# Performance work log

Measured on AMD Instinct MI355X. Metric: run time of the kernel, lower is better.

## Reference

```python
import jax, jax.numpy as jnp
import numpy as np

B, N, E, H, L, T, IN = 32, 512, 32768, 64, 2, 2, 8
TAU = 0.5


def setup_inputs() -> dict:
    key = jax.random.key(0)
    ks = jax.random.split(key, 32)
    f = lambda i, shape, s=0.05: jax.random.normal(ks[i], shape, jnp.float32) * s
    u = jax.random.uniform(ks[3], (B, E, T), jnp.float32, 1e-6, 1.0 - 1e-6)
    return {
        "inputs": f(0, (B, N, IN), 1.0),
        "hidden": f(1, (B, N, H), 1.0),
        "edge_logits": f(2, (B, E, T), 1.0),
        "gumbel": -jnp.log(-jnp.log(u)),  # standard Gumbel noise (deterministic here)
        "send_edges": jax.random.randint(ks[4], (E,), 0, N),
        "recv_edges": jax.random.randint(ks[5], (E,), 0, N),
        "W1": f(6, (L, T, H, 2 * H)), "b1": f(7, (L, T, H)),
        "W2": f(8, (L, T, H, H)), "b2": f(9, (L, T, H)),
        "Whr": f(10, (H, L * H)), "Whi": f(11, (H, L * H)), "Whh": f(12, (H, L * H)),
        "Wir": f(13, (H, IN)), "bir": f(14, (H,)),
        "Wii": f(15, (H, IN)), "bii": f(16, (H,)),
        "Win": f(17, (H, IN)), "bin_w": f(18, (H,)),
        "Wm1": f(19, (H, H)), "bm1": f(20, (H,)),
        "Wm2": f(21, (H, H)), "bm2": f(22, (H,)),
        "Wdf": f(23, (N, N * H), 0.005), "bdf": f(24, (N,)),
        "Wloc": f(25, (N, N * H), 0.005), "bloc": f(26, (N,)),
        "Wscale": f(27, (N, N * H), 0.005), "bscale": f(28, (N,)),
    }


def _lin(x, W, b):
    return jnp.einsum('...i,oi->...o', x, W) + b


def reference(inputs, hidden, edge_logits, gumbel, send_edges, recv_edges,
              W1, b1, W2, b2, Whr, Whi, Whh,
              Wir, bir, Wii, bii, Win, bin_w,
              Wm1, bm1, Wm2, bm2,
              Wdf, bdf, Wloc, bloc, Wscale, bscale):
    # hard gumbel-softmax (straight-through)
    y_soft = jax.nn.softmax((edge_logits + gumbel) / TAU, axis=-1)
    y_hard = jax.nn.one_hot(jnp.argmax(y_soft, axis=-1), T, dtype=y_soft.dtype)
    edges = jax.lax.stop_gradient(y_hard - y_soft) + y_soft  # [B,E,T]

    # normalized receiver degree (zeros -> 1), as in edge2node_mat / degree
    deg = jnp.zeros((N,), jnp.float32).at[recv_edges].add(1.0)
    deg = jnp.where(deg == 0, 1.0, deg)

    hidden_ = hidden
    aggs = []
    norm = float(T)  # skip_first_edge_type=False
    for k in range(L):
        pre = jnp.concatenate([hidden_[:, recv_edges], hidden_[:, send_edges]], axis=-1)  # [B,E,2H]
        all_msgs = jnp.zeros((B, E, H), pre.dtype)
        for t in range(T):  # per-edge-type tanh MLP (eval mode: dropout off)
            m = jnp.tanh(jnp.einsum('bef,hf->beh', pre, W1[k, t]) + b1[k, t])
            m = jnp.tanh(jnp.einsum('beh,gh->beg', m, W2[k, t]) + b2[k, t])
            all_msgs = all_msgs + m * edges[:, :, t:t + 1] / norm
        # scatter-mean onto receiver nodes (= normalized edge2node matmul)
        agg = jnp.zeros((B, N, H), all_msgs.dtype).at[:, recv_edges].add(all_msgs) / deg[None, :, None]
        hidden_ = agg
        aggs.append(agg)
    agg = jnp.concatenate(aggs, axis=-1)  # [B,N,L*H]

    r = jax.nn.sigmoid(_lin(inputs, Wir, bir) + jnp.einsum('bnf,of->bno', agg, Whr))
    i = jax.nn.sigmoid(_lin(inputs, Wii, bii) + jnp.einsum('bnf,of->bno', agg, Whi))
    n = jnp.tanh(_lin(inputs, Win, bin_w) + r * jnp.einsum('bnf,of->bno', agg, Whh))
    hidden_new = (1.0 - i) * n + i * hidden  # [B,N,H]

    pred = _lin(jax.nn.relu(_lin(hidden_new, Wm1, bm1)), Wm2, bm2)
    flat = pred.reshape(B, -1)  # [B, N*H]
    df = 2.0 + jax.nn.softplus(flat @ Wdf.T + bdf)      # StudentT domain maps
    loc = flat @ Wloc.T + bloc
    scale = jax.nn.softplus(flat @ Wscale.T + bscale)
    return df, loc, scale, hidden_new, edges
```

## Files before the change

### kernel.cpp

```cpp
#include <hip/hip_runtime.h>

#define B_  32
#define N_  512
#define E_  32768
#define H_  64
#define L_  2
#define T_  2
#define IN_ 8

typedef __attribute__((ext_vector_type(4))) float f32x4;
typedef __attribute__((ext_vector_type(8))) short bf16x8;
typedef __attribute__((ext_vector_type(4))) short s16x4;
typedef __attribute__((ext_vector_type(4))) unsigned u32x4;

__device__ __forceinline__ short f2bf(float f){
  unsigned u = __float_as_uint(f);
  u += 0x7FFFu + ((u >> 16) & 1u);
  return (short)(u >> 16);
}
__device__ __forceinline__ float bf2f(short s){
  return __uint_as_float(((unsigned)(unsigned short)s) << 16);
}
__device__ __forceinline__ bf16x8 pack8(f32x4 a, f32x4 b){
  bf16x8 r;
  r[0]=f2bf(a[0]); r[1]=f2bf(a[1]); r[2]=f2bf(a[2]); r[3]=f2bf(a[3]);
  r[4]=f2bf(b[0]); r[5]=f2bf(b[1]); r[6]=f2bf(b[2]); r[7]=f2bf(b[3]);
  return r;
}
__device__ __forceinline__ float lo16f(unsigned u){ return __uint_as_float(u << 16); }
__device__ __forceinline__ float hi16f(unsigned u){ return __uint_as_float(u & 0xffff0000u); }

__device__ __forceinline__ float fast_tanh(float x){
  float e = __builtin_amdgcn_exp2f(x * 2.8853900817779268f);
  float r = __builtin_amdgcn_rcpf(e + 1.0f);
  return __builtin_fmaf(-2.0f, r, 1.0f);
}
__device__ __forceinline__ float fast_sigm(float x){
  return __builtin_amdgcn_rcpf(1.0f + __builtin_amdgcn_exp2f(x * -1.4426950408889634f));
}
__device__ __forceinline__ float softplus_f(float x){
  return fmaxf(x, 0.0f) + log1pf(__expf(-fabsf(x)));
}

__global__ void k_edges(const float* __restrict__ logits, const float* __restrict__ gum,
                        float* __restrict__ edges_out, unsigned char* __restrict__ type_out){
  int i = blockIdx.x * 256 + threadIdx.x;
  if(i >= B_ * E_) return;
  float l0 = logits[2*i]   + gum[2*i];
  float l1 = logits[2*i+1] + gum[2*i+1];
  int t = (l1 > l0) ? 1 : 0;
  edges_out[2*i]   = t ? 0.f : 1.f;
  edges_out[2*i+1] = t ? 1.f : 0.f;
  type_out[i] = (unsigned char)t;
}

__global__ void k_hist(const int* __restrict__ recvE, int* __restrict__ hist){
  int e = blockIdx.x * 256 + threadIdx.x;
  if(e < E_) atomicAdd(&hist[recvE[e]], 1);
}
__global__ void k_scan(const int* __restrict__ hist, int* __restrict__ row_start,
                       float* __restrict__ deg){
  __shared__ int a[512], bbuf[512];
  int t = threadIdx.x;
  int h = hist[t];
  a[t] = h;
  __syncthreads();
  int* cur = a; int* nxt = bbuf;
  for(int off = 1; off < 512; off <<= 1){
    int v = cur[t] + (t >= off ? cur[t - off] : 0);
    nxt[t] = v;
    __syncthreads();
    int* tmp = cur; cur = nxt; nxt = tmp;
  }
  row_start[t] = cur[t] - h;
  if(t == 0) row_start[512] = E_;
  deg[t] = (h == 0) ? 1.0f : (float)h;
}

__global__ void k_hist2(const int* __restrict__ recvE, const unsigned char* __restrict__ typ,
                        int* __restrict__ n0){
  __shared__ int lh[512];
  int b = blockIdx.y, tid = threadIdx.x;
  lh[tid] = 0; lh[tid + 256] = 0;
  __syncthreads();
  int e0 = blockIdx.x * 2048;
  for(int k = 0; k < 8; ++k){
    int e = e0 + k*256 + tid;
    if(typ[(size_t)b*E_ + e] == 0) atomicAdd(&lh[recvE[e]], 1);
  }
  __syncthreads();
  if(lh[tid])       atomicAdd(&n0[b*512 + tid],       lh[tid]);
  if(lh[tid + 256]) atomicAdd(&n0[b*512 + tid + 256], lh[tid + 256]);
}
__global__ void k_scan2(const int* __restrict__ n0, const int* __restrict__ row_start,
                        int* __restrict__ stt){
  __shared__ int a[512], bbuf[512];
  __shared__ int tot;
  int b = blockIdx.x, t = threadIdx.x;
  int h = n0[b*512 + t];
  a[t] = h;
  __syncthreads();
  int* cur = a; int* nxt = bbuf;
  for(int off = 1; off < 512; off <<= 1){
    int v = cur[t] + (t >= off ? cur[t - off] : 0);
    nxt[t] = v;
    __syncthreads();
    int* tmp = cur; cur = nxt; nxt = tmp;
  }
  if(t == 511) tot = cur[511];
  __syncthreads();
  int excl = cur[t] - h;
  stt[(b*2    )*513 + t] = excl;
  stt[(b*2 + 1)*513 + t] = tot + row_start[t] - excl;
  if(t == 0){ stt[(b*2)*513 + 512] = tot; stt[(b*2+1)*513 + 512] = E_; }
}
__global__ void k_perm2(const int* __restrict__ recvE, const unsigned char* __restrict__ typ,
                        const int* __restrict__ stt, int* __restrict__ cur0,
                        int* __restrict__ cur1, unsigned short* __restrict__ perm2){
  int i = blockIdx.x * 256 + threadIdx.x;
  int b = i >> 15, e = i & (E_ - 1);
  int r = recvE[e];
  int pos;
  if(typ[i] == 0) pos = stt[(b*2  )*513 + r] + atomicAdd(&cur0[b*512 + r], 1);
  else            pos = stt[(b*2+1)*513 + r] + atomicAdd(&cur1[b*512 + r], 1);
  perm2[(size_t)b*E_ + pos] = (unsigned short)e;
}

__launch_bounds__(256, 2)
__global__ void k_prep(const float* __restrict__ hid,
                       const float* __restrict__ W1, const float* __restrict__ b1,
                       unsigned short* __restrict__ P, int layer){
  __shared__ __align__(16) short WT[256 * 64];
  __shared__ float bias[256];
  __shared__ float hidl[32 * 64];

  const int tid = threadIdx.x;
  const int b   = blockIdx.y;
  const int nbase = blockIdx.x * 32;
  const float* W1k = W1 + layer * (T_ * H_ * 2 * H_);

  {
    int col = tid, slot = col >> 6, h = col & 63;
    int t = slot & 1, prt = slot >> 1;
    const float* src = W1k + t*8192 + h*128 + prt*64;
#pragma unroll
    for(int u = 0; u < 8; ++u){
      bf16x8 v = pack8(*(const f32x4*)(src + u*8), *(const f32x4*)(src + u*8 + 4));
      int bo = col*128 + ((u*16) ^ ((col & 7) << 4));
      *(bf16x8*)((char*)WT + bo) = v;
    }
    bias[col] = (slot < 2) ? b1[layer*128 + t*64 + h] : 0.0f;
  }
  {
    const float* src = hid + ((size_t)b*N_ + nbase)*H_;
    ((f32x4*)hidl)[tid]       = ((const f32x4*)src)[tid];
    ((f32x4*)hidl)[tid + 256] = ((const f32x4*)src)[tid + 256];
  }
  __syncthreads();

  const int col = tid;
  for(int n = 0; n < 32; ++n){
    const float* hrow = hidl + n*64;
    float acc = bias[col];
#pragma unroll
    for(int u = 0; u < 8; ++u){
      int bo = col*128 + ((u*16) ^ ((col & 7) << 4));
      bf16x8 wv = *(const bf16x8*)((const char*)WT + bo);
#pragma unroll
      for(int i = 0; i < 8; ++i) acc += hrow[u*8 + i] * bf2f(wv[i]);
    }
    P[(((size_t)b*N_ + nbase + n) << 8) + col] = (unsigned short)f2bf(acc);
  }
}

__launch_bounds__(256, 5)
__global__ void k_msg(const unsigned short* __restrict__ P,
                      const float* __restrict__ W2, const float* __restrict__ b2,
                      const int* __restrict__ recvE, const int* __restrict__ sendE,
                      const unsigned short* __restrict__ perm2,
                      const int* __restrict__ stt, const float* __restrict__ deg,
                      float* __restrict__ agg, int layer){
  __shared__ __align__(16) short m1_lds[2][64 * 64];
  __shared__ float acc[8][64];
  __shared__ float b2_lds[128];
  __shared__ short rl_lds[2][64];

  const int tid  = threadIdx.x;
  const int w    = tid >> 6, lane = tid & 63;
  const int l15  = lane & 15, l4 = lane >> 4;
  const int b    = blockIdx.y;
  const int nodeBase = blockIdx.x * 8;

  const float* W2k = W2 + layer * (T_ * H_ * H_);

  if(tid < 128) b2_lds[tid] = b2[layer*128 + tid];
  acc[tid >> 6][tid & 63] = 0.0f;
  { int t2 = tid + 256; acc[t2 >> 6][t2 & 63] = 0.0f; }

  bf16x8 B2f[2][2];
#pragma unroll
  for(int t = 0; t < 2; ++t)
#pragma unroll
    for(int ks = 0; ks < 2; ++ks){
      const float* p = W2k + (t*64 + w*16 + l15)*64 + ks*32 + l4*8;
      B2f[t][ks] = pack8(*(const f32x4*)p, *(const f32x4*)(p+4));
    }

  const int gcol = w*16 + l15;
  const unsigned short* permB = perm2 + (size_t)b * E_;
  const int* sttB = stt + b*2*513;
  const int s0a = sttB[nodeBase],       s1a = sttB[nodeBase + 8];
  const int s0b = sttB[513 + nodeBase], s1b = sttB[513 + nodeBase + 8];
  const int nt0 = (s1a - s0a + 63) >> 6;
  const int nt  = nt0 + ((s1b - s0b + 63) >> 6);

  const int el = tid >> 2, part = tid & 3;
  const int h0 = part * 16;
  const int bo0 = el*128 + ((h0*2)      ^ ((el & 7) << 4));
  const int bo1 = el*128 + ((h0*2 + 16) ^ ((el & 7) << 4));

#define TILE_SL(t, sv, lv) { if((t) < nt0){ sv = s0a + (t)*64 + el; lv = s1a; } \
                             else { sv = s0b + ((t) - nt0)*64 + el; lv = s1b; } }

  u32x4 G0 = {}, G1 = {}, G2 = {}, G3 = {};
  int rl_cur = 255, eidA = 0;
  bool v_cur = false;

  if(nt > 0){
    int s, lim;
    TILE_SL(0, s, lim);
    bool v0 = s < lim;
    int e0 = v0 ? (int)permB[s] : 0;
    int rv0 = v0 ? recvE[e0] : 0;
    int sd0 = v0 ? sendE[e0] : 0;
    if(v0){
      int sg0 = (nt0 == 0) ? 1 : 0;
      const unsigned short* pr = P + (((size_t)b*N_ + rv0) << 8) + sg0*64 + h0;
      const unsigned short* ps = P + (((size_t)b*N_ + sd0) << 8) + (2 + sg0)*64 + h0;
      G0 = *(const u32x4*)pr; G1 = *(const u32x4*)(pr + 8);
      G2 = *(const u32x4*)ps; G3 = *(const u32x4*)(ps + 8);
    }
    rl_cur = v0 ? (rv0 - nodeBase) : 255;
    v_cur = v0;
    TILE_SL(1, s, lim);
    eidA = (s < lim) ? (int)permB[s] : 0;
  }

  for(int ti = 0; ti < nt; ++ti){
    const int c = ti & 1;
    if(v_cur){
      unsigned q0[4], q1[4];
#pragma unroll
      for(int j = 0; j < 4; ++j){
        unsigned t0 = (unsigned)(unsigned short)f2bf(fast_tanh(lo16f(G0[j]) + lo16f(G2[j])));
        unsigned t1 = (unsigned)(unsigned short)f2bf(fast_tanh(hi16f(G0[j]) + hi16f(G2[j])));
        q0[j] = t0 | (t1 << 16);
        unsigned t2 = (unsigned)(unsigned short)f2bf(fast_tanh(lo16f(G1[j]) + lo16f(G3[j])));
        unsigned t3 = (unsigned)(unsigned short)f2bf(fast_tanh(hi16f(G1[j]) + hi16f(G3[j])));
        q1[j] = t2 | (t3 << 16);
      }
      *(u32x4*)((char*)m1_lds[c] + bo0) = (u32x4){q0[0], q0[1], q0[2], q0[3]};
      *(u32x4*)((char*)m1_lds[c] + bo1) = (u32x4){q1[0], q1[1], q1[2], q1[3]};
    }else{
      u32x4 z = {};
      *(u32x4*)((char*)m1_lds[c] + bo0) = z;
      *(u32x4*)((char*)m1_lds[c] + bo1) = z;
    }
    if(part == 0) rl_lds[c][el] = (short)rl_cur;
    __syncthreads();

    int rvN = 0, sdN = 0; bool vN;
    {
      int s, lim;
      TILE_SL(ti + 1, s, lim);
      vN = s < lim;
      if(vN){ rvN = recvE[eidA]; sdN = sendE[eidA]; }
      TILE_SL(ti + 2, s, lim);
      eidA = (s < lim) ? (int)permB[s] : 0;
    }

    const int sg = (ti >= nt0) ? 1 : 0;
    f32x4 C2[4];
    { float bv = b2_lds[sg*64 + gcol];
#pragma unroll
      for(int ef = 0; ef < 4; ++ef) C2[ef] = (f32x4){bv, bv, bv, bv}; }
#pragma unroll
    for(int ks = 0; ks < 2; ++ks){
#pragma unroll
      for(int ef = 0; ef < 4; ++ef){
        int e = ef*16 + l15;
        int byteoff = e*128 + (((ks*32 + l4*8)*2) ^ ((e & 7) << 4));
        bf16x8 A = *(const bf16x8*)((const char*)m1_lds[c] + byteoff);
        C2[ef] = __builtin_amdgcn_mfma_f32_16x16x32_bf16(A, B2f[sg][ks], C2[ef], 0, 0, 0);
      }
    }
    {
      int prl = -1; float pend = 0.f;
#pragma unroll
      for(int ef = 0; ef < 4; ++ef){
        s16x4 rl4 = *(const s16x4*)&rl_lds[c][ef*16 + l4*4];
#pragma unroll
        for(int r = 0; r < 4; ++r){
          int rl = rl4[r];
          if(rl != prl){
            if(prl >= 0) atomicAdd(&acc[prl][gcol], pend);
            pend = 0.f;
            prl = (rl == 255) ? -1 : rl;
          }
          if(rl != 255) pend += fast_tanh(C2[ef][r]);
        }
      }
      if(prl >= 0) atomicAdd(&acc[prl][gcol], pend);
    }

    if(vN){
      const int sgN = (ti + 1 >= nt0) ? 1 : 0;
      const unsigned short* pr = P + (((size_t)b*N_ + rvN) << 8) + sgN*64 + h0;
      const unsigned short* ps = P + (((size_t)b*N_ + sdN) << 8) + (2 + sgN)*64 + h0;
      G0 = *(const u32x4*)pr; G1 = *(const u32x4*)(pr + 8);
      G2 = *(const u32x4*)ps; G3 = *(const u32x4*)(ps + 8);
    }else{
      G0 = (u32x4){}; G1 = (u32x4){}; G2 = (u32x4){}; G3 = (u32x4){};
    }
    rl_cur = vN ? (rvN - nodeBase) : 255;
    v_cur = vN;
  }
#undef TILE_SL
  __syncthreads();

#pragma unroll
  for(int q = 0; q < 2; ++q){
    int idx = tid + q*256;
    int rl = idx >> 6, g = idx & 63;
    int node = nodeBase + rl;
    agg[(((size_t)b*N_ + node) << 6) + g] = acc[rl][g] * 0.5f / deg[node];
  }
}

__launch_bounds__(256, 2)
__global__ void k_gru(const float* __restrict__ x, const float* __restrict__ hid,
                      const float* __restrict__ agg0, const float* __restrict__ agg1,
                      const float* __restrict__ Whr, const float* __restrict__ Whi,
                      const float* __restrict__ Whh,
                      const float* __restrict__ Wir, const float* __restrict__ bir,
                      const float* __restrict__ Wii, const float* __restrict__ bii,
                      const float* __restrict__ Win, const float* __restrict__ binw,
                      float* __restrict__ hnew){
  __shared__ short WhrT[128*64], WhiT[128*64], WhhT[128*64];
  __shared__ float WxT[3][8*64];
  __shared__ float bias[3][64];
  __shared__ float agg_lds[4][128];

  int tid = threadIdx.x;
  for(int s = tid; s < 8192; s += 256){
    int g = s >> 7, f = s & 127;
    WhrT[f*64+g] = f2bf(Whr[s]);
    WhiT[f*64+g] = f2bf(Whi[s]);
    WhhT[f*64+g] = f2bf(Whh[s]);
  }
  for(int s = tid; s < 512; s += 256){
    int g = s >> 3, j = s & 7;
    WxT[0][j*64+g] = Wir[s]; WxT[1][j*64+g] = Wii[s]; WxT[2][j*64+g] = Win[s];
  }
  if(tid < 64){ bias[0][tid] = bir[tid]; bias[1][tid] = bii[tid]; bias[2][tid] = binw[tid]; }
  __syncthreads();

  int w = tid >> 6, lane = tid & 63;
  for(int j = 0; j < 8; ++j){
    int id = blockIdx.x*32 + j*4 + w;
    size_t base = (size_t)id * 64;
    agg_lds[w][lane]      = agg0[base + lane];
    agg_lds[w][64 + lane] = agg1[base + lane];

    float ar = bias[0][lane], ai = bias[1][lane], an = bias[2][lane], ah = 0.f;
    const float* xp = x + (size_t)id * 8;
#pragma unroll
    for(int jj = 0; jj < 8; ++jj){
      float xv = xp[jj];
      ar += xv * WxT[0][jj*64+lane];
      ai += xv * WxT[1][jj*64+lane];
      an += xv * WxT[2][jj*64+lane];
    }
#pragma unroll 4
    for(int f = 0; f < 128; ++f){
      float av = agg_lds[w][f];
      ar += av * bf2f(WhrT[f*64+lane]);
      ai += av * bf2f(WhiT[f*64+lane]);
      ah += av * bf2f(WhhT[f*64+lane]);
    }
    float r  = fast_sigm(ar);
    float ii = fast_sigm(ai);
    float ng = fast_tanh(an + r * ah);
    float ho = hid[base + lane];
    hnew[base + lane] = (1.0f - ii) * ng + ii * ho;
  }
}

__launch_bounds__(256, 2)
__global__ void k_pred(const float* __restrict__ hnew,
                       const float* __restrict__ Wm1, const float* __restrict__ bm1,
                       const float* __restrict__ Wm2, const float* __restrict__ bm2,
                       unsigned short* __restrict__ flatbf){
  __shared__ float W1T[64*64], W2T[64*64];
  __shared__ float bias1[64], bias2[64];
  __shared__ float h_lds[4][64], t_lds[4][64];
  int tid = threadIdx.x;
  for(int s = tid; s < 4096; s += 256){
    int g = s >> 6, h = s & 63;
    W1T[h*64+g] = Wm1[s];
    W2T[h*64+g] = Wm2[s];
  }
  if(tid < 64){ bias1[tid] = bm1[tid]; bias2[tid] = bm2[tid]; }
  __syncthreads();

  int w = tid >> 6, lane = tid & 63;
  for(int j = 0; j < 8; ++j){
    int id = blockIdx.x*32 + j*4 + w;
    size_t base = (size_t)id * 64;
    h_lds[w][lane] = hnew[base + lane];
    float a = bias1[lane];
#pragma unroll 4
    for(int h = 0; h < 64; ++h) a += h_lds[w][h] * W1T[h*64+lane];
    a = fmaxf(a, 0.0f);
    t_lds[w][lane] = a;
    float p = bias2[lane];
#pragma unroll 4
    for(int h = 0; h < 64; ++h) p += t_lds[w][h] * W2T[h*64+lane];
    flatbf[base + lane] = (unsigned short)f2bf(p);
  }
}

__launch_bounds__(256, 6)
__global__ void k_out(const float* __restrict__ Wdf, const float* __restrict__ Wloc,
                      const float* __restrict__ Wsc,
                      const unsigned short* __restrict__ flatbf,
                      float* __restrict__ pacc){
  const int bid = blockIdx.x;
  const int mt  = bid >> 5;
  const int kb  = bid & 31;
  const int row0 = mt * 32;
  const int mat  = row0 >> 9;
  const int rloc = row0 & 511;
  const float* W = (mat == 0) ? Wdf : (mat == 1) ? Wloc : Wsc;

  const int tid = threadIdx.x, w = tid >> 6, lane = tid & 63;
  const int l15 = lane & 15, l4 = lane >> 4;
  const float* wp = W + (size_t)(rloc + (w & 1)*16 + l15)*32768 + kb*1024 + l4*8;
  const unsigned short* fp = flatbf + (size_t)((w >> 1)*16 + l15)*32768 + kb*1024 + l4*8;

  f32x4 acc0 = {}, acc1 = {};
#pragma unroll 4
  for(int ks = 0; ks < 32; ks += 2){
    f32x4 a0 = *(const f32x4*)(wp + ks*32);
    f32x4 a1 = *(const f32x4*)(wp + ks*32 + 4);
    bf16x8 Bv0 = *(const bf16x8*)(fp + ks*32);
    f32x4 a2 = *(const f32x4*)(wp + ks*32 + 32);
    f32x4 a3 = *(const f32x4*)(wp + ks*32 + 36);
    bf16x8 Bv1 = *(const bf16x8*)(fp + ks*32 + 32);
    acc0 = __builtin_amdgcn_mfma_f32_16x16x32_bf16(pack8(a0, a1), Bv0, acc0, 0, 0, 0);
    acc1 = __builtin_amdgcn_mfma_f32_16x16x32_bf16(pack8(a2, a3), Bv1, acc1, 0, 0, 0);
  }
#pragma unroll
  for(int r = 0; r < 4; ++r){
    int grow = row0 + (w & 1)*16 + l4*4 + r;
    atomicAdd(&pacc[grow*32 + (w >> 1)*16 + l15], acc0[r] + acc1[r]);
  }
}

__global__ void k_fin(const float* __restrict__ pacc,
                      const float* __restrict__ bdf, const float* __restrict__ bloc,
                      const float* __restrict__ bsc, float* __restrict__ out){
  int i = blockIdx.x*256 + threadIdx.x;
  int mat = i >> 14;
  int rem = i & 16383;
  int b = rem >> 9, og = rem & 511;
  float s = pacc[(mat*512 + og)*32 + b];
  s += (mat == 0 ? bdf : mat == 1 ? bloc : bsc)[og];
  float res = (mat == 0) ? 2.0f + softplus_f(s) : (mat == 1) ? s : softplus_f(s);
  out[i] = res;
}

extern "C" void kernel_launch(void* const* d_in, const int* in_sizes, int n_in,
                              void* d_out, int out_size, void* d_ws, size_t ws_size,
                              hipStream_t stream){
  (void)in_sizes; (void)n_in; (void)out_size; (void)ws_size;
  const float* inputs = (const float*)d_in[0];
  const float* hidden = (const float*)d_in[1];
  const float* elog   = (const float*)d_in[2];
  const float* gum    = (const float*)d_in[3];
  const int*   sendE  = (const int*)  d_in[4];
  const int*   recvE  = (const int*)  d_in[5];
  const float* W1   = (const float*)d_in[6];
  const float* b1   = (const float*)d_in[7];
  const float* W2   = (const float*)d_in[8];
  const float* b2   = (const float*)d_in[9];
  const float* Whr  = (const float*)d_in[10];
  const float* Whi  = (const float*)d_in[11];
  const float* Whh  = (const float*)d_in[12];
  const float* Wir  = (const float*)d_in[13]; const float* bir  = (const float*)d_in[14];
  const float* Wii  = (const float*)d_in[15]; const float* bii  = (const float*)d_in[16];
  const float* Win  = (const float*)d_in[17]; const float* binw = (const float*)d_in[18];
  const float* Wm1  = (const float*)d_in[19]; const float* bm1  = (const float*)d_in[20];
  const float* Wm2  = (const float*)d_in[21]; const float* bm2  = (const float*)d_in[22];
  const float* Wdf  = (const float*)d_in[23]; const float* bdf  = (const float*)d_in[24];
  const float* Wloc = (const float*)d_in[25]; const float* bloc = (const float*)d_in[26];
  const float* Wsc  = (const float*)d_in[27]; const float* bsc  = (const float*)d_in[28];

  float* out       = (float*)d_out;
  float* out_hid   = out + 49152;
  float* out_edges = out + 1097728;

  char* ws = (char*)d_ws;
  float* agg0 = (float*)(ws);
  float* agg1 = (float*)(ws + 4194304);
  unsigned short* P = (unsigned short*)(ws + 8388608);
  unsigned short* flatbf = (unsigned short*)(ws + 8388608);
  unsigned short* perm2 = (unsigned short*)(ws + 16777216);
  unsigned char* typ = (unsigned char*)(ws + 18874368);
  int*   hist      = (int*)(ws + 19922944);
  int*   row_start = (int*)(ws + 19924992);
  float* deg       = (float*)(ws + 19929088);
  int*   n0        = (int*)(ws + 19931136);
  int*   cur0      = (int*)(ws + 19996672);
  int*   cur1      = (int*)(ws + 20062208);
  int*   stt       = (int*)(ws + 20127744);
  float* pacc      = agg0;

  hipMemsetAsync(hist, 0, 2048, stream);
  hipMemsetAsync(n0, 0, 3*65536, stream);

  k_edges<<<4096, 256, 0, stream>>>(elog, gum, out_edges, typ);
  k_hist<<<128, 256, 0, stream>>>(recvE, hist);
  k_scan<<<1, 512, 0, stream>>>(hist, row_start, deg);
  k_hist2<<<dim3(16, 32), 256, 0, stream>>>(recvE, typ, n0);
  k_scan2<<<32, 512, 0, stream>>>(n0, row_start, stt);
  k_perm2<<<4096, 256, 0, stream>>>(recvE, typ, stt, cur0, cur1, perm2);

  k_prep<<<dim3(16, 32), 256, 0, stream>>>(hidden, W1, b1, P, 0);
  k_msg<<<dim3(64, 32), 256, 0, stream>>>(P, W2, b2, recvE, sendE,
                                          perm2, stt, deg, agg0, 0);
  k_prep<<<dim3(16, 32), 256, 0, stream>>>(agg0, W1, b1, P, 1);
  k_msg<<<dim3(64, 32), 256, 0, stream>>>(P, W2, b2, recvE, sendE,
                                          perm2, stt, deg, agg1, 1);

  k_gru<<<512, 256, 0, stream>>>(inputs, hidden, agg0, agg1,
                                 Whr, Whi, Whh, Wir, bir, Wii, bii, Win, binw, out_hid);
  k_pred<<<512, 256, 0, stream>>>(out_hid, Wm1, bm1, Wm2, bm2, flatbf);
  hipMemsetAsync(pacc, 0, 1536*32*4, stream);
  k_out<<<1536, 256, 0, stream>>>(Wdf, Wloc, Wsc, flatbf, pacc);
  k_fin<<<192, 256, 0, stream>>>(pacc, bdf, bloc, bsc, out);
}
```

Measured before the change: 481.0 us.

## Use hardware packed bf16 conversion, vectorize edge kernel, raise k_msg occupancy

Replaces the software round-to-nearest bf16 conversion with the v_cvt_pk_bf16_f32 instruction in the message tanh path and in the output projection's weight packing, cutting per-element ALU work. Vectorizes k_edges to handle two edges per thread with 128-bit loads and stores, and halves its grid. Raises the k_msg launch-bounds occupancy hint from 5 to 8, which caps registers per thread and may cause spills.

```diff
diff --git a/kernel.cpp b/kernel.cpp
--- a/kernel.cpp
+++ b/kernel.cpp
@@ -27,6 +27,19 @@
   r[4]=f2bf(b[0]); r[5]=f2bf(b[1]); r[6]=f2bf(b[2]); r[7]=f2bf(b[3]);
   return r;
 }
+__device__ __forceinline__ unsigned cvt_pk_bf16(float lo, float hi){
+  unsigned r;
+  asm("v_cvt_pk_bf16_f32 %0, %1, %2" : "=v"(r) : "v"(lo), "v"(hi));
+  return r;
+}
+__device__ __forceinline__ bf16x8 pack8cvt(f32x4 a, f32x4 b){
+  union { u32x4 u; bf16x8 h; } r;
+  r.u[0] = cvt_pk_bf16(a[0], a[1]);
+  r.u[1] = cvt_pk_bf16(a[2], a[3]);
+  r.u[2] = cvt_pk_bf16(b[0], b[1]);
+  r.u[3] = cvt_pk_bf16(b[2], b[3]);
+  return r.h;
+}
 __device__ __forceinline__ float lo16f(unsigned u){ return __uint_as_float(u << 16); }
 __device__ __forceinline__ float hi16f(unsigned u){ return __uint_as_float(u & 0xffff0000u); }
 
@@ -44,14 +57,15 @@
 
 __global__ void k_edges(const float* __restrict__ logits, const float* __restrict__ gum,
                         float* __restrict__ edges_out, unsigned char* __restrict__ type_out){
-  int i = blockIdx.x * 256 + threadIdx.x;
-  if(i >= B_ * E_) return;
-  float l0 = logits[2*i]   + gum[2*i];
-  float l1 = logits[2*i+1] + gum[2*i+1];
-  int t = (l1 > l0) ? 1 : 0;
-  edges_out[2*i]   = t ? 0.f : 1.f;
-  edges_out[2*i+1] = t ? 1.f : 0.f;
-  type_out[i] = (unsigned char)t;
+  int i2 = blockIdx.x * 256 + threadIdx.x;
+  f32x4 lg = *(const f32x4*)(logits + (size_t)i2*4);
+  f32x4 gm = *(const f32x4*)(gum    + (size_t)i2*4);
+  int ta = (lg[1] + gm[1] > lg[0] + gm[0]) ? 1 : 0;
+  int tb = (lg[3] + gm[3] > lg[2] + gm[2]) ? 1 : 0;
+  f32x4 o = { ta ? 0.f : 1.f, ta ? 1.f : 0.f, tb ? 0.f : 1.f, tb ? 1.f : 0.f };
+  *(f32x4*)(edges_out + (size_t)i2*4) = o;
+  unsigned short tw = (unsigned short)(ta | (tb << 8));
+  *(unsigned short*)(type_out + (size_t)i2*2) = tw;
 }
 
 __global__ void k_hist(const int* __restrict__ recvE, int* __restrict__ hist){
@@ -173,7 +187,7 @@
   }
 }
 
-__launch_bounds__(256, 5)
+__launch_bounds__(256, 8)
 __global__ void k_msg(const unsigned short* __restrict__ P,
                       const float* __restrict__ W2, const float* __restrict__ b2,
                       const int* __restrict__ recvE, const int* __restrict__ sendE,
@@ -252,12 +266,10 @@
       unsigned q0[4], q1[4];
 #pragma unroll
       for(int j = 0; j < 4; ++j){
-        unsigned t0 = (unsigned)(unsigned short)f2bf(fast_tanh(lo16f(G0[j]) + lo16f(G2[j])));
-        unsigned t1 = (unsigned)(unsigned short)f2bf(fast_tanh(hi16f(G0[j]) + hi16f(G2[j])));
-        q0[j] = t0 | (t1 << 16);
-        unsigned t2 = (unsigned)(unsigned short)f2bf(fast_tanh(lo16f(G1[j]) + lo16f(G3[j])));
-        unsigned t3 = (unsigned)(unsigned short)f2bf(fast_tanh(hi16f(G1[j]) + hi16f(G3[j])));
-        q1[j] = t2 | (t3 << 16);
+        q0[j] = cvt_pk_bf16(fast_tanh(lo16f(G0[j]) + lo16f(G2[j])),
+                            fast_tanh(hi16f(G0[j]) + hi16f(G2[j])));
+        q1[j] = cvt_pk_bf16(fast_tanh(lo16f(G1[j]) + lo16f(G3[j])),
+                            fast_tanh(hi16f(G1[j]) + hi16f(G3[j])));
       }
       *(u32x4*)((char*)m1_lds[c] + bo0) = (u32x4){q0[0], q0[1], q0[2], q0[3]};
       *(u32x4*)((char*)m1_lds[c] + bo1) = (u32x4){q1[0], q1[1], q1[2], q1[3]};
@@ -457,8 +469,8 @@
     f32x4 a2 = *(const f32x4*)(wp + ks*32 + 32);
     f32x4 a3 = *(const f32x4*)(wp + ks*32 + 36);
     bf16x8 Bv1 = *(const bf16x8*)(fp + ks*32 + 32);
-    acc0 = __builtin_amdgcn_mfma_f32_16x16x32_bf16(pack8(a0, a1), Bv0, acc0, 0, 0, 0);
-    acc1 = __builtin_amdgcn_mfma_f32_16x16x32_bf16(pack8(a2, a3), Bv1, acc1, 0, 0, 0);
+    acc0 = __builtin_amdgcn_mfma_f32_16x16x32_bf16(pack8cvt(a0, a1), Bv0, acc0, 0, 0, 0);
+    acc1 = __builtin_amdgcn_mfma_f32_16x16x32_bf16(pack8cvt(a2, a3), Bv1, acc1, 0, 0, 0);
   }
 #pragma unroll
   for(int r = 0; r < 4; ++r){
@@ -529,7 +541,7 @@
   hipMemsetAsync(hist, 0, 2048, stream);
   hipMemsetAsync(n0, 0, 3*65536, stream);
 
-  k_edges<<<4096, 256, 0, stream>>>(elog, gum, out_edges, typ);
+  k_edges<<<2048, 256, 0, stream>>>(elog, gum, out_edges, typ);
   k_hist<<<128, 256, 0, stream>>>(recvE, hist);
   k_scan<<<1, 512, 0, stream>>>(hist, row_start, deg);
   k_hist2<<<dim3(16, 32), 256, 0, stream>>>(recvE, typ, n0);
```

New measurement: 1.475 ms. 3.07x slower.
